# Kernel optimization log

Measured on AMD Instinct MI355X. Metric: run time of the kernel, lower is better.

The kernel has to match this reference:

```python
import jax, jax.numpy as jnp
import numpy as np
from jax import lax

B, L, H = 16, 96, 128  # batch, encoder_input_size (seq/channels), hidden_size


def _same_pad(k):
    # torch Conv2d padding='same' (stride=1, dilation=1): left = (k-1)//2, extra on right
    t = k - 1
    return (t // 2, t - t // 2)


def setup_inputs() -> dict:
    key = jax.random.key(0)
    ks = jax.random.split(key, 10)
    return {
        "hidden": jax.random.normal(ks[0], (B, H), jnp.float32),
        "encoder_outputs": jax.random.normal(ks[1], (B, L, H), jnp.float32),
        "coverage": jax.random.uniform(ks[2], (B, L), jnp.float32),
        # attnConv: Conv2d(L, L, (H, H)) weight [out,in,kh,kw]
        "attn_conv_w": jax.random.normal(ks[3], (L, L, H, H), jnp.float32) * 0.02,
        "attn_conv_b": jax.random.normal(ks[4], (L,), jnp.float32) * 0.02,
        # cvgConv: Conv2d(L, L, (1, H))
        "cvg_conv_w": jax.random.normal(ks[5], (L, L, 1, H), jnp.float32) * 0.02,
        "cvg_conv_b": jax.random.normal(ks[6], (L,), jnp.float32) * 0.02,
        # decoderAttnLinear: Linear(H, H)
        "dec_w": jax.random.normal(ks[7], (H, H), jnp.float32) * 0.02,
        "dec_b": jax.random.normal(ks[8], (H,), jnp.float32) * 0.02,
        # v: Parameter [batch, hidden]
        "v": jax.random.normal(ks[9], (B, H), jnp.float32) * 0.1,
    }


def reference(hidden, encoder_outputs, coverage, attn_conv_w, attn_conv_b,
              cvg_conv_w, cvg_conv_b, dec_w, dec_b, v):
    dn = ("NCHW", "OIHW", "NCHW")
    # encoder features: conv over [B, L, 1, H] with (H, H) kernel, 'same' padding -> [B, L, 1, H]
    x = encoder_outputs[:, :, None, :]
    enc_f = lax.conv_general_dilated(
        x, attn_conv_w, (1, 1), [_same_pad(H), _same_pad(H)], dimension_numbers=dn
    ) + attn_conv_b[None, :, None, None]
    # decoder features: Linear(hidden) -> [B, 1, 1, H]
    dec_f = (hidden @ dec_w.T + dec_b)[:, None, None, :]
    # coverage features: conv over [B, L, 1, 1] with (1, H) kernel, 'same' -> [B, L, 1, 1]
    c = coverage[:, :, None, None]
    cvg_f = lax.conv_general_dilated(
        c, cvg_conv_w, (1, 1), [(0, 0), _same_pad(H)], dimension_numbers=dn
    ) + cvg_conv_b[None, :, None, None]
    # additive attention: tanh of summed features, project with v, softmax over L
    feats = jnp.tanh((enc_f + dec_f + cvg_f).reshape(B, L, H))
    scores = jnp.einsum("blh,bh->bl", feats, v)
    attn = jax.nn.softmax(scores, axis=1)
    new_coverage = coverage + attn
    context = jnp.einsum("bl,blh->bh", attn, encoder_outputs)
    return context, attn, new_coverage
```

## Files before the change

kernel.cpp:

```cpp
#include <hip/hip_runtime.h>
#include <hip/hip_bf16.h>
#include <math.h>

#define BB 16
#define LL 96
#define HH 128

typedef __attribute__((ext_vector_type(8))) short short8;
typedef __attribute__((ext_vector_type(4))) float f32x4;

#define WS_W    0
#define WS_E    589824
#define WS_DEC  983040
#define WS_CVG  985088
#define WS_SC   986624
#define WS_P    988160

__global__ __launch_bounds__(256) void prep_kernel(
        const float* __restrict__ hidden,
        const float* __restrict__ enc,
        const float* __restrict__ coverage,
        const float* __restrict__ attn_w,
        const float* __restrict__ cvg_w,
        const float* __restrict__ cvg_b,
        const float* __restrict__ dec_w,
        const float* __restrict__ dec_b,
        float* __restrict__ ws) {
    const int bid = blockIdx.x;
    const int tid = threadIdx.x;
    if (bid < 96) {
        const int i = bid;
        unsigned short* wout = (unsigned short*)(ws + WS_W);
        for (int idx = tid; idx < LL * HH; idx += 256) {
            const int o = idx >> 7, e = idx & 127;
            const int esrc = e ^ ((o & 7) << 3);
            float v = attn_w[(((size_t)o * LL + i) * HH + 63) * HH + esrc];
            __hip_bfloat16 h = __float2bfloat16(v);
            wout[(size_t)i * LL * HH + idx] = *(unsigned short*)&h;
        }
    } else if (bid < 112) {
        const int b = bid - 96;
        float* eout = ws + WS_E + (size_t)b * LL * 256;
        for (int idx = tid; idx < LL * 256; idx += 256) {
            const int i = idx >> 8, t = idx & 255;
            eout[idx] = (t >= 63 && t < 191) ? enc[((size_t)b * LL + i) * HH + (t - 63)] : 0.f;
        }
    } else {
        const int b = bid - 112;
        __shared__ float hid[HH];
        __shared__ float cov[LL];
        if (tid < HH) hid[tid] = hidden[b * HH + tid];
        if (tid < LL) cov[tid] = coverage[b * LL + tid];
        __syncthreads();
        if (tid < HH) {
            float acc = dec_b[tid];
            for (int k = 0; k < HH; ++k) acc += hid[k] * dec_w[tid * HH + k];
            ws[WS_DEC + b * HH + tid] = acc;
        } else if (tid < HH + LL) {
            const int t = tid - HH;
            float a2 = cvg_b[t];
            for (int i2 = 0; i2 < LL; ++i2)
                a2 += cov[i2] * cvg_w[((size_t)t * LL + i2) * HH + 63];
            ws[WS_CVG + b * LL + t] = a2;
        }
    }
}

__global__ __launch_bounds__(256) void mfma_kernel(float* __restrict__ ws) {
    const int kc = blockIdx.x;
    const int b  = blockIdx.y;
    const int tid  = threadIdx.x;
    const int lane = tid & 63;
    const int wg   = tid >> 6;
    const int lo   = lane & 15;
    const int hi   = lane >> 4;

    __shared__ __align__(16) short Abuf[LL * HH];
    __shared__ __align__(16) float Ebuf[256];

    f32x4 acc[6][2];
#pragma unroll
    for (int a = 0; a < 6; ++a)
#pragma unroll
        for (int c = 0; c < 2; ++c) acc[a][c] = f32x4{0.f, 0.f, 0.f, 0.f};

    const short* wsrc = (const short*)(ws + WS_W);
    const float* esrc = ws + WS_E + (size_t)b * LL * 256;

    for (int ii = 0; ii < 3; ++ii) {
        const int ig = kc * 3 + ii;
        __syncthreads();
        {
            const short8* s8 = (const short8*)(wsrc + (size_t)ig * LL * HH);
            short8* d8 = (short8*)Abuf;
#pragma unroll
            for (int t = 0; t < 6; ++t) d8[tid + t * 256] = s8[tid + t * 256];
            if (tid < 64)
                ((float4*)Ebuf)[tid] = ((const float4*)(esrc + ig * 256))[tid];
        }
        __syncthreads();

#pragma unroll
        for (int s = 0; s < 4; ++s) {
            short8 af[6];
#pragma unroll
            for (int ot = 0; ot < 6; ++ot) {
                const int o = ot * 16 + lo;
                const int idx8 = o * 16 + (((s << 2) + hi) ^ (o & 7));
                af[ot] = ((const short8*)Abuf)[idx8];
            }
#pragma unroll
            for (int wt = 0; wt < 2; ++wt) {
                const int t0 = s * 32 + hi * 8 + wg * 32 + wt * 16 + lo;
                union { short8 s8; __hip_bfloat16 h[8]; } bf;
#pragma unroll
                for (int j = 0; j < 8; ++j) bf.h[j] = __float2bfloat16(Ebuf[t0 + j]);
#pragma unroll
                for (int ot = 0; ot < 6; ++ot)
                    acc[ot][wt] = __builtin_amdgcn_mfma_f32_16x16x32_bf16(
                        af[ot], bf.s8, acc[ot][wt], 0, 0, 0);
            }
        }
    }

    float* dst = ws + WS_P + ((size_t)kc * BB + b) * LL * HH;
#pragma unroll
    for (int ot = 0; ot < 6; ++ot)
#pragma unroll
        for (int wt = 0; wt < 2; ++wt)
#pragma unroll
            for (int r = 0; r < 4; ++r) {
                const int o = ot * 16 + hi * 4 + r;
                const int w = wg * 32 + wt * 16 + lo;
                dst[o * HH + w] = acc[ot][wt][r];
            }
}

__global__ __launch_bounds__(128) void reduce_kernel(
        const float* __restrict__ attn_b,
        const float* __restrict__ vvec,
        float* __restrict__ ws) {
    const int o = blockIdx.x;
    const int b = blockIdx.y;
    const int h = threadIdx.x;
    const float* p = ws + WS_P + (size_t)b * LL * HH + o * HH + h;
    float sum = 0.f;
#pragma unroll
    for (int kc = 0; kc < 32; ++kc) sum += p[(size_t)kc * BB * LL * HH];
    float ef = sum + attn_b[o] + ws[WS_DEC + b * HH + h] + ws[WS_CVG + b * LL + o];
    float s = tanhf(ef) * vvec[b * HH + h];
#pragma unroll
    for (int off = 32; off > 0; off >>= 1) s += __shfl_down(s, off, 64);
    __shared__ float r2[2];
    if ((h & 63) == 0) r2[h >> 6] = s;
    __syncthreads();
    if (h == 0) ws[WS_SC + b * LL + o] = r2[0] + r2[1];
}

__global__ void finalize_kernel(const float* __restrict__ ws_scores,
                                const float* __restrict__ coverage,
                                const float* __restrict__ enc,
                                float* __restrict__ out) {
    int b = blockIdx.x;
    int t = threadIdx.x;
    __shared__ float sc[LL];
    __shared__ float at[LL];
    if (t < LL) sc[t] = ws_scores[b * LL + t];
    __syncthreads();

    float mx = -1e30f;
    for (int l = 0; l < LL; ++l) mx = fmaxf(mx, sc[l]);
    float sum = 0.f;
    for (int l = 0; l < LL; ++l) sum += expf(sc[l] - mx);

    if (t < LL) {
        float a = expf(sc[t] - mx) / sum;
        at[t] = a;
        out[BB * HH + b * LL + t] = a;
        out[BB * HH + BB * LL + b * LL + t] = coverage[b * LL + t] + a;
    }
    __syncthreads();

    float ctx = 0.f;
    for (int l = 0; l < LL; ++l) ctx += at[l] * enc[(b * LL + l) * HH + t];
    out[b * HH + t] = ctx;
}

extern "C" void kernel_launch(void* const* d_in, const int* in_sizes, int n_in,
                              void* d_out, int out_size, void* d_ws, size_t ws_size,
                              hipStream_t stream) {
    const float* hidden   = (const float*)d_in[0];
    const float* enc      = (const float*)d_in[1];
    const float* coverage = (const float*)d_in[2];
    const float* attn_w   = (const float*)d_in[3];
    const float* attn_b   = (const float*)d_in[4];
    const float* cvg_w    = (const float*)d_in[5];
    const float* cvg_b    = (const float*)d_in[6];
    const float* dec_w    = (const float*)d_in[7];
    const float* dec_b    = (const float*)d_in[8];
    const float* vvec     = (const float*)d_in[9];
    float* out = (float*)d_out;
    float* ws = (float*)d_ws;

    prep_kernel<<<128, 256, 0, stream>>>(hidden, enc, coverage, attn_w,
                                         cvg_w, cvg_b, dec_w, dec_b, ws);
    mfma_kernel<<<dim3(32, BB), 256, 0, stream>>>(ws);
    reduce_kernel<<<dim3(LL, BB), 128, 0, stream>>>(attn_b, vvec, ws);
    finalize_kernel<<<BB, HH, 0, stream>>>(ws + WS_SC, coverage, enc, out);
}
```

Measured before the change: 49.08 us.

## Restructure conv pipeline: prelaid bf16 operands, double-buffered MFMA, fp16 partials, fused reduce

The prep kernel now writes the weight slices directly in MFMA fragment order and pre-converts the padded encoder rows to bf16 in an even/odd-shifted pair layout, so the MFMA kernel loads A fragments straight from global memory into registers instead of staging them through LDS. The MFMA kernel uses 512 threads with 16 k-chunks, double-buffers the encoder row and A fragments across 6 input channels, and reduces the four k-quarter waves through LDS before writing partials as fp16. The separate reduce and finalize kernels are merged into one per-batch kernel that sums the 16 partials, applies tanh and v, and does the softmax and context, saving a launch. Storing partials in fp16 lowers precision, and the merged reduce runs on only 16 blocks.

Result: slower. 79.71 us (+62.4%).

```diff
diff --git a/kernel.cpp b/kernel.cpp
--- a/kernel.cpp
+++ b/kernel.cpp
@@ -1,5 +1,6 @@
 #include <hip/hip_runtime.h>
 #include <hip/hip_bf16.h>
+#include <hip/hip_fp16.h>
 #include <math.h>
 
 #define BB 16
@@ -9,12 +10,11 @@
 typedef __attribute__((ext_vector_type(8))) short short8;
 typedef __attribute__((ext_vector_type(4))) float f32x4;
 
-#define WS_W    0
-#define WS_E    589824
-#define WS_DEC  983040
-#define WS_CVG  985088
-#define WS_SC   986624
-#define WS_P    988160
+#define WS_W_OFF   0
+#define WS_E_OFF   2359296
+#define WS_DEC_OFF 4030464
+#define WS_CVG_OFF 4038656
+#define WS_P_OFF   4044800
 
 __global__ __launch_bounds__(256) void prep_kernel(
         const float* __restrict__ hidden,
@@ -25,28 +25,52 @@
         const float* __restrict__ cvg_b,
         const float* __restrict__ dec_w,
         const float* __restrict__ dec_b,
-        float* __restrict__ ws) {
+        char* __restrict__ wsb) {
     const int bid = blockIdx.x;
     const int tid = threadIdx.x;
     if (bid < 96) {
-        const int i = bid;
-        unsigned short* wout = (unsigned short*)(ws + WS_W);
-        for (int idx = tid; idx < LL * HH; idx += 256) {
-            const int o = idx >> 7, e = idx & 127;
-            const int esrc = e ^ ((o & 7) << 3);
-            float v = attn_w[(((size_t)o * LL + i) * HH + 63) * HH + esrc];
-            __hip_bfloat16 h = __float2bfloat16(v);
-            wout[(size_t)i * LL * HH + idx] = *(unsigned short*)&h;
+        const int ig = bid;
+        unsigned short* wout = (unsigned short*)(wsb + WS_W_OFF);
+        for (int base = tid * 8; base < LL * HH; base += 256 * 8) {
+            const int o = base >> 7, k = base & 127;
+            const int kq = k >> 5, h2 = (k >> 3) & 3;
+            const int ot = o >> 4, l2 = o & 15;
+            const float* src = attn_w + ((size_t)(o * LL + ig) * 16384 + 8064 + k);
+            union { unsigned short us[8]; uint4 u4; } tm;
+#pragma unroll
+            for (int j = 0; j < 8; ++j) {
+                __hip_bfloat16 h = __float2bfloat16(src[j]);
+                tm.us[j] = *(unsigned short*)&h;
+            }
+            uint4* dst = (uint4*)(wout + ((size_t)((ig * 4 + kq) * 6 + ot) * 512
+                                          + (h2 * 16 + l2) * 8));
+            *dst = tm.u4;
         }
     } else if (bid < 112) {
         const int b = bid - 96;
-        float* eout = ws + WS_E + (size_t)b * LL * 256;
-        for (int idx = tid; idx < LL * 256; idx += 256) {
-            const int i = idx >> 8, t = idx & 255;
-            eout[idx] = (t >= 63 && t < 191) ? enc[((size_t)b * LL + i) * HH + (t - 63)] : 0.f;
+        unsigned int* eout = (unsigned int*)(wsb + WS_E_OFF) + (size_t)b * LL * 272;
+        const float* esrc = enc + (size_t)b * LL * HH;
+        for (int i = 0; i < LL; ++i) {
+            for (int c = tid; c < 272; c += 256) {
+                int t0 = -1, t1 = -1;
+                if (c < 128) { t0 = 2 * c; t1 = 2 * c + 1; }
+                else if (c >= 129 && c < 257) { int i2 = c - 129; t0 = 2 * i2 + 1; t1 = 2 * i2 + 2; }
+                unsigned int lo16 = 0, hi16 = 0;
+                if (t0 >= 63 && t0 < 191) {
+                    __hip_bfloat16 h = __float2bfloat16(esrc[i * HH + t0 - 63]);
+                    lo16 = *(unsigned short*)&h;
+                }
+                if (t1 >= 63 && t1 < 191) {
+                    __hip_bfloat16 h = __float2bfloat16(esrc[i * HH + t1 - 63]);
+                    hi16 = *(unsigned short*)&h;
+                }
+                eout[i * 272 + c] = lo16 | (hi16 << 16);
+            }
         }
     } else {
         const int b = bid - 112;
+        float* decf = (float*)(wsb + WS_DEC_OFF);
+        float* cvgf = (float*)(wsb + WS_CVG_OFF);
         __shared__ float hid[HH];
         __shared__ float cov[LL];
         if (tid < HH) hid[tid] = hidden[b * HH + tid];
@@ -55,135 +79,179 @@
         if (tid < HH) {
             float acc = dec_b[tid];
             for (int k = 0; k < HH; ++k) acc += hid[k] * dec_w[tid * HH + k];
-            ws[WS_DEC + b * HH + tid] = acc;
+            decf[b * HH + tid] = acc;
         } else if (tid < HH + LL) {
             const int t = tid - HH;
             float a2 = cvg_b[t];
             for (int i2 = 0; i2 < LL; ++i2)
                 a2 += cov[i2] * cvg_w[((size_t)t * LL + i2) * HH + 63];
-            ws[WS_CVG + b * LL + t] = a2;
-        }
-    }
-}
-
-__global__ __launch_bounds__(256) void mfma_kernel(float* __restrict__ ws) {
+            cvgf[b * LL + t] = a2;
+        }
+    }
+}
+
+__global__ __launch_bounds__(512, 2) void mfma_kernel(char* __restrict__ wsb) {
     const int kc = blockIdx.x;
     const int b  = blockIdx.y;
-    const int tid  = threadIdx.x;
-    const int lane = tid & 63;
-    const int wg   = tid >> 6;
-    const int lo   = lane & 15;
-    const int hi   = lane >> 4;
-
-    __shared__ __align__(16) short Abuf[LL * HH];
-    __shared__ __align__(16) float Ebuf[256];
-
-    f32x4 acc[6][2];
-#pragma unroll
-    for (int a = 0; a < 6; ++a)
-#pragma unroll
-        for (int c = 0; c < 2; ++c) acc[a][c] = f32x4{0.f, 0.f, 0.f, 0.f};
-
-    const short* wsrc = (const short*)(ws + WS_W);
-    const float* esrc = ws + WS_E + (size_t)b * LL * 256;
-
-    for (int ii = 0; ii < 3; ++ii) {
-        const int ig = kc * 3 + ii;
+    const int tid    = threadIdx.x;
+    const int lane   = tid & 63;
+    const int waveid = tid >> 6;
+    const int lo = lane & 15;
+    const int hi = lane >> 4;
+    const int kq    = waveid >> 1;
+    const int whalf = waveid & 1;
+
+    __shared__ unsigned int rowbuf[2][272];
+    __shared__ float red[6][1024];
+
+    const unsigned short* Wp = (const unsigned short*)(wsb + WS_W_OFF);
+    const unsigned int* Ep = (const unsigned int*)(wsb + WS_E_OFF)
+                             + ((size_t)b * LL + kc * 6) * 272;
+    __half* Pp = (__half*)(wsb + WS_P_OFF);
+
+    f32x4 acc[6][4];
+#pragma unroll
+    for (int ot = 0; ot < 6; ++ot)
+#pragma unroll
+        for (int wt = 0; wt < 4; ++wt) acc[ot][wt] = f32x4{0.f, 0.f, 0.f, 0.f};
+
+    short8 afA[6], afB[6];
+    uint4 sreg;
+
+    auto stageIssue = [&](int r) {
+        if (tid < 68) sreg = *(const uint4*)(Ep + r * 272 + tid * 4);
+    };
+    auto stageWrite = [&](int bufi) {
+        if (tid < 68) *(uint4*)&rowbuf[bufi][tid * 4] = sreg;
+    };
+    auto loadA = [&](int r, short8* af) {
+        const unsigned short* base =
+            Wp + (size_t)(((kc * 6 + r) * 4 + kq) * 6) * 512 + lane * 8;
+#pragma unroll
+        for (int ot = 0; ot < 6; ++ot)
+            af[ot] = *(const short8*)(base + ot * 512);
+    };
+    auto compute = [&](int bufi, short8* af) {
+        const unsigned int* row = rowbuf[bufi];
+#pragma unroll
+        for (int wt = 0; wt < 4; ++wt) {
+            const int t0 = kq * 32 + whalf * 64 + wt * 16 + hi * 8 + lo;
+            const unsigned int* arr = row + ((lo & 1) ? 129 : 0) + (t0 >> 1);
+            union { uint4 u; short8 s; } bf;
+            bf.u.x = arr[0]; bf.u.y = arr[1]; bf.u.z = arr[2]; bf.u.w = arr[3];
+#pragma unroll
+            for (int ot = 0; ot < 6; ++ot)
+                acc[ot][wt] = __builtin_amdgcn_mfma_f32_16x16x32_bf16(
+                    af[ot], bf.s, acc[ot][wt], 0, 0, 0);
+        }
+    };
+
+    stageIssue(0); loadA(0, afA); stageWrite(0);
+    __syncthreads();
+    stageIssue(1); loadA(1, afB); compute(0, afA); stageWrite(1);
+    __syncthreads();
+    stageIssue(2); loadA(2, afA); compute(1, afB); stageWrite(0);
+    __syncthreads();
+    stageIssue(3); loadA(3, afB); compute(0, afA); stageWrite(1);
+    __syncthreads();
+    stageIssue(4); loadA(4, afA); compute(1, afB); stageWrite(0);
+    __syncthreads();
+    stageIssue(5); loadA(5, afB); compute(0, afA); stageWrite(1);
+    __syncthreads();
+    compute(1, afB);
+
+#pragma unroll
+    for (int ot = 0; ot < 6; ++ot) {
         __syncthreads();
-        {
-            const short8* s8 = (const short8*)(wsrc + (size_t)ig * LL * HH);
-            short8* d8 = (short8*)Abuf;
-#pragma unroll
-            for (int t = 0; t < 6; ++t) d8[tid + t * 256] = s8[tid + t * 256];
-            if (tid < 64)
-                ((float4*)Ebuf)[tid] = ((const float4*)(esrc + ig * 256))[tid];
+        if (waveid >= 2) {
+            const int slot = waveid - 2;
+#pragma unroll
+            for (int wt = 0; wt < 4; ++wt)
+                *(f32x4*)&red[slot][(wt * 64 + lane) * 4] = acc[ot][wt];
         }
         __syncthreads();
-
-#pragma unroll
-        for (int s = 0; s < 4; ++s) {
-            short8 af[6];
-#pragma unroll
-            for (int ot = 0; ot < 6; ++ot) {
-                const int o = ot * 16 + lo;
-                const int idx8 = o * 16 + (((s << 2) + hi) ^ (o & 7));
-                af[ot] = ((const short8*)Abuf)[idx8];
+        if (waveid < 2) {
+#pragma unroll
+            for (int s = 0; s < 3; ++s)
+#pragma unroll
+                for (int wt = 0; wt < 4; ++wt)
+                    acc[ot][wt] += *(const f32x4*)&red[s * 2 + whalf][(wt * 64 + lane) * 4];
+#pragma unroll
+            for (int wt = 0; wt < 4; ++wt) {
+                const int w  = whalf * 64 + wt * 16 + lo;
+                const int o0 = ot * 16 + hi * 4;
+                __half2 p01 = __floats2half2_rn(acc[ot][wt][0], acc[ot][wt][1]);
+                __half2 p23 = __floats2half2_rn(acc[ot][wt][2], acc[ot][wt][3]);
+                __half2* dst = (__half2*)(Pp + (((size_t)(kc * BB + b) * HH + w) * LL + o0));
+                dst[0] = p01; dst[1] = p23;
             }
-#pragma unroll
-            for (int wt = 0; wt < 2; ++wt) {
-                const int t0 = s * 32 + hi * 8 + wg * 32 + wt * 16 + lo;
-                union { short8 s8; __hip_bfloat16 h[8]; } bf;
-#pragma unroll
-                for (int j = 0; j < 8; ++j) bf.h[j] = __float2bfloat16(Ebuf[t0 + j]);
-#pragma unroll
-                for (int ot = 0; ot < 6; ++ot)
-                    acc[ot][wt] = __builtin_amdgcn_mfma_f32_16x16x32_bf16(
-                        af[ot], bf.s8, acc[ot][wt], 0, 0, 0);
-            }
-        }
-    }
-
-    float* dst = ws + WS_P + ((size_t)kc * BB + b) * LL * HH;
-#pragma unroll
-    for (int ot = 0; ot < 6; ++ot)
-#pragma unroll
-        for (int wt = 0; wt < 2; ++wt)
-#pragma unroll
-            for (int r = 0; r < 4; ++r) {
-                const int o = ot * 16 + hi * 4 + r;
-                const int w = wg * 32 + wt * 16 + lo;
-                dst[o * HH + w] = acc[ot][wt][r];
-            }
-}
-
-__global__ __launch_bounds__(128) void reduce_kernel(
+        }
+    }
+}
+
+__global__ __launch_bounds__(256) void reduceF_kernel(
         const float* __restrict__ attn_b,
         const float* __restrict__ vvec,
-        float* __restrict__ ws) {
-    const int o = blockIdx.x;
-    const int b = blockIdx.y;
-    const int h = threadIdx.x;
-    const float* p = ws + WS_P + (size_t)b * LL * HH + o * HH + h;
-    float sum = 0.f;
-#pragma unroll
-    for (int kc = 0; kc < 32; ++kc) sum += p[(size_t)kc * BB * LL * HH];
-    float ef = sum + attn_b[o] + ws[WS_DEC + b * HH + h] + ws[WS_CVG + b * LL + o];
-    float s = tanhf(ef) * vvec[b * HH + h];
-#pragma unroll
-    for (int off = 32; off > 0; off >>= 1) s += __shfl_down(s, off, 64);
-    __shared__ float r2[2];
-    if ((h & 63) == 0) r2[h >> 6] = s;
-    __syncthreads();
-    if (h == 0) ws[WS_SC + b * LL + o] = r2[0] + r2[1];
-}
-
-__global__ void finalize_kernel(const float* __restrict__ ws_scores,
-                                const float* __restrict__ coverage,
-                                const float* __restrict__ enc,
-                                float* __restrict__ out) {
-    int b = blockIdx.x;
-    int t = threadIdx.x;
-    __shared__ float sc[LL];
-    __shared__ float at[LL];
-    if (t < LL) sc[t] = ws_scores[b * LL + t];
-    __syncthreads();
-
+        const float* __restrict__ coverage,
+        const float* __restrict__ enc,
+        const char* __restrict__ wsb,
+        float* __restrict__ out) {
+    const int b = blockIdx.x;
+    const int t = threadIdx.x;
+    const int w = t >> 1, oh = t & 1;
+    const __half* Pp = (const __half*)(wsb + WS_P_OFF);
+    const float* dec = (const float*)(wsb + WS_DEC_OFF);
+    const float* cvg = (const float*)(wsb + WS_CVG_OFF);
+
+    __shared__ float sA[LL], sC[LL];
+    __shared__ float scr[LL][130];
+    __shared__ float sc[LL], at[LL];
+
+    if (t < LL) { sA[t] = attn_b[t]; sC[t] = cvg[b * LL + t]; }
+    __syncthreads();
+
+    float sum[48];
+#pragma unroll
+    for (int j = 0; j < 48; ++j) sum[j] = 0.f;
+    for (int kc = 0; kc < 16; ++kc) {
+        const __half2* p2 = (const __half2*)(Pp + (((size_t)(kc * BB + b) * HH + w) * LL + oh * 48));
+#pragma unroll
+        for (int q = 0; q < 24; ++q) {
+            __half2 h = p2[q];
+            sum[2 * q]     += __low2float(h);
+            sum[2 * q + 1] += __high2float(h);
+        }
+    }
+    const float dv = dec[b * HH + w];
+    const float vv = vvec[b * HH + w];
+#pragma unroll
+    for (int j = 0; j < 48; ++j) {
+        const int o = oh * 48 + j;
+        scr[o][w] = tanhf(sum[j] + sA[o] + sC[o] + dv) * vv;
+    }
+    __syncthreads();
+    if (t < LL) {
+        float s = 0.f;
+        for (int ww = 0; ww < HH; ++ww) s += scr[t][ww];
+        sc[t] = s;
+    }
+    __syncthreads();
     float mx = -1e30f;
     for (int l = 0; l < LL; ++l) mx = fmaxf(mx, sc[l]);
-    float sum = 0.f;
-    for (int l = 0; l < LL; ++l) sum += expf(sc[l] - mx);
-
+    float den = 0.f;
+    for (int l = 0; l < LL; ++l) den += expf(sc[l] - mx);
     if (t < LL) {
-        float a = expf(sc[t] - mx) / sum;
+        float a = expf(sc[t] - mx) / den;
         at[t] = a;
         out[BB * HH + b * LL + t] = a;
         out[BB * HH + BB * LL + b * LL + t] = coverage[b * LL + t] + a;
     }
     __syncthreads();
-
-    float ctx = 0.f;
-    for (int l = 0; l < LL; ++l) ctx += at[l] * enc[(b * LL + l) * HH + t];
-    out[b * HH + t] = ctx;
+    if (t < HH) {
+        float c = 0.f;
+        for (int l = 0; l < LL; ++l) c += at[l] * enc[((size_t)b * LL + l) * HH + t];
+        out[b * HH + t] = c;
+    }
 }
 
 extern "C" void kernel_launch(void* const* d_in, const int* in_sizes, int n_in,
@@ -200,11 +268,10 @@
     const float* dec_b    = (const float*)d_in[8];
     const float* vvec     = (const float*)d_in[9];
     float* out = (float*)d_out;
-    float* ws = (float*)d_ws;
+    char* wsb = (char*)d_ws;
 
     prep_kernel<<<128, 256, 0, stream>>>(hidden, enc, coverage, attn_w,
-                                         cvg_w, cvg_b, dec_w, dec_b, ws);
-    mfma_kernel<<<dim3(32, BB), 256, 0, stream>>>(ws);
-    reduce_kernel<<<dim3(LL, BB), 128, 0, stream>>>(attn_b, vvec, ws);
-    finalize_kernel<<<BB, HH, 0, stream>>>(ws + WS_SC, coverage, enc, out);
-}
+                                         cvg_w, cvg_b, dec_w, dec_b, wsb);
+    mfma_kernel<<<dim3(16, BB), 512, 0, stream>>>(wsb);
+    reduceF_kernel<<<BB, 256, 0, stream>>>(attn_b, vvec, coverage, enc, wsb, out);
+}
```
